# Kernel optimization log

Measured on AMD Instinct MI355X. Metric: run time of the kernel, lower is better.

The kernel has to match this reference:

```python
import jax, jax.numpy as jnp
import numpy as np

DIM = 1024
HEADS = 16
HEAD_DIM = DIM // HEADS


def setup_inputs() -> dict:
    key = jax.random.key(0)
    ks = jax.random.split(key, 7)
    scale = 1.0 / np.sqrt(DIM)
    x = jax.random.normal(ks[0], (2, 2048, DIM), dtype=jnp.float32)
    Wq = jax.random.uniform(ks[1], (DIM, DIM), jnp.float32, -scale, scale)
    bq = jax.random.uniform(ks[2], (DIM,), jnp.float32, -scale, scale)
    Wk = jax.random.uniform(ks[3], (DIM, DIM), jnp.float32, -scale, scale)
    bk = jax.random.uniform(ks[4], (DIM,), jnp.float32, -scale, scale)
    Wv = jax.random.uniform(ks[5], (DIM, DIM), jnp.float32, -scale, scale)
    bv = jax.random.uniform(ks[6], (DIM,), jnp.float32, -scale, scale)
    return {"x": x, "Wq": Wq, "bq": bq, "Wk": Wk, "bk": bk, "Wv": Wv, "bv": bv}


def reference(x, Wq, bq, Wk, bk, Wv, bv):
    b, s, _ = x.shape
    # torch Linear: y = x @ W.T + b
    q = (x @ Wq.T + bq).reshape(b, s, HEADS, HEAD_DIM)
    k = (x @ Wk.T + bk).reshape(b, s, HEADS, HEAD_DIM)
    v = (x @ Wv.T + bv).reshape(b, s, HEADS, HEAD_DIM)
    # scores: (b, s, z, h), softmax over z (key axis = axis 2)
    scores = jnp.einsum('bshd,bzhd->bszh', q, k) / jnp.sqrt(jnp.float32(HEAD_DIM))
    attention = jax.nn.softmax(scores, axis=2)
    output = jnp.einsum('bzhd,bszh->bshd', v, attention)
    return output
```

## Files before the change

kernel.cpp:

```cpp
#include <hip/hip_runtime.h>
#include <hip/hip_bf16.h>

typedef unsigned short u16;
typedef __attribute__((ext_vector_type(8))) __bf16 bf16x8;
typedef __attribute__((ext_vector_type(4))) float f32x4;
typedef __attribute__((ext_vector_type(8))) u16 u16x8;

#define BATCH 2
#define SEQ   2048
#define DIM   1024
#define HEADS 16
#define HDIM  64

#define QSCALE 0.18033688011112042f

__device__ __forceinline__ float bf2f(u16 u) {
  union { unsigned int u; float f; } v; v.u = ((unsigned int)u) << 16; return v.f;
}
__device__ __forceinline__ u16 f2bf(float f) {
  union { float f; unsigned int u; } v; v.f = f;
  unsigned int r = v.u + 0x7fffu + ((v.u >> 16) & 1u);
  return (u16)(r >> 16);
}
__device__ __forceinline__ unsigned int pk2(float a, float b) {
  union { __hip_bfloat162 h2; unsigned int u; } v;
  v.h2 = __float22bfloat162_rn(float2{a, b});
  return v.u;
}

__device__ __forceinline__ void async16(u16* lds, const u16* g) {
  __builtin_amdgcn_global_load_lds(
      (__attribute__((address_space(1))) void*)(void*)(g),
      (__attribute__((address_space(3))) void*)(lds), 16, 0, 0);
}

#define XG  524288
#define WG  131072
extern "C" __global__ __launch_bounds__(256)
void convert_all(const float* __restrict__ x,  const float* __restrict__ wq,
                 const float* __restrict__ wk, const float* __restrict__ wv,
                 u16* __restrict__ xbf, u16* __restrict__ wbf)
{
  const int g = blockIdx.x * 256 + threadIdx.x;
  const float* src; u16* dst; size_t off;
  if (g < XG)               { src = x;  dst = xbf;                 off = (size_t)g; }
  else if (g < XG + WG)     { src = wq; dst = wbf;                 off = (size_t)(g - XG); }
  else if (g < XG + 2 * WG) { src = wk; dst = wbf + DIM * DIM;     off = (size_t)(g - XG - WG); }
  else                      { src = wv; dst = wbf + 2 * DIM * DIM; off = (size_t)(g - XG - 2 * WG); }
  f32x4 a = *(const f32x4*)(src + off * 8);
  f32x4 b = *(const f32x4*)(src + off * 8 + 4);
  u16x8 o;
#pragma unroll
  for (int i = 0; i < 4; ++i) { o[i] = f2bf(a[i]); o[4 + i] = f2bf(b[i]); }
  *(u16x8*)(dst + off * 8) = o;
}

extern "C" __global__ __launch_bounds__(256)
void qkv_gemm(const u16* __restrict__ xbf, const u16* __restrict__ wbf,
              const float* __restrict__ bq, const float* __restrict__ bk,
              const float* __restrict__ bv,
              u16* __restrict__ qo, u16* __restrict__ ko, u16* __restrict__ vto)
{
  __shared__ alignas(16) u16 Albs[128 * 64];
  __shared__ alignas(16) u16 Blbs[128 * 64];

  const int which = blockIdx.z;
  const u16* Wb = wbf + (size_t)which * DIM * DIM;
  const float* bias = (which == 0) ? bq : (which == 1) ? bk : bv;

  const int lane = threadIdx.x & 63;
  const int wave = threadIdx.x >> 6;
  const int l16  = lane & 15;
  const int quad = lane >> 4;
  const int r8   = lane >> 3;
  const int sl   = lane & 7;
  const int jsw  = sl ^ (r8 & 7);
  const int e7   = l16 & 7;

  const int mBase = blockIdx.y * 128;
  const int nBase = blockIdx.x * 128;
  const int mw = (wave >> 1) * 64;
  const int nw = (wave & 1) * 64;

  f32x4 acc[4][4] = {};

  for (int k0 = 0; k0 < DIM; k0 += 64) {
#pragma unroll
    for (int p = 0; p < 4; ++p) {
      const int i = wave * 4 + p;
      async16(&Albs[i * 512], xbf + (size_t)(mBase + i * 8 + r8) * DIM + k0 + jsw * 8);
      async16(&Blbs[i * 512], Wb  + (size_t)(nBase + i * 8 + r8) * DIM + k0 + jsw * 8);
    }
    asm volatile("s_waitcnt vmcnt(0)" ::: "memory");
    __syncthreads();

    bf16x8 af[4][2], bfr[4][2];
#pragma unroll
    for (int i = 0; i < 4; ++i)
#pragma unroll
      for (int ks = 0; ks < 2; ++ks) {
        af[i][ks]  = *(const bf16x8*)&Albs[(mw + i * 16 + l16) * 64 + ((ks * 4 + quad) ^ e7) * 8];
        bfr[i][ks] = *(const bf16x8*)&Blbs[(nw + i * 16 + l16) * 64 + ((ks * 4 + quad) ^ e7) * 8];
      }
#pragma unroll
    for (int ks = 0; ks < 2; ++ks)
#pragma unroll
      for (int mi = 0; mi < 4; ++mi)
#pragma unroll
        for (int ni = 0; ni < 4; ++ni)
          acc[mi][ni] = __builtin_amdgcn_mfma_f32_16x16x32_bf16(af[mi][ks], bfr[ni][ks], acc[mi][ni], 0, 0, 0);
    __syncthreads();
  }

  const float oscale = (which == 0) ? QSCALE : 1.0f;
#pragma unroll
  for (int ni = 0; ni < 4; ++ni) {
    const int n = nBase + nw + ni * 16 + l16;
    const float bval = bias[n];
    const int h = n >> 6, d = n & 63;
#pragma unroll
    for (int mi = 0; mi < 4; ++mi) {
#pragma unroll
      for (int r = 0; r < 4; ++r) {
        const int m = mBase + mw + mi * 16 + quad * 4 + r;
        const int bi = m >> 11, s = m & 2047;
        const u16 val = f2bf((acc[mi][ni][r] + bval) * oscale);
        if (which == 2) {
          vto[((size_t)(bi * HEADS + h) * HDIM + d) * SEQ + s] = val;
        } else {
          u16* dst = (which == 0) ? qo : ko;
          dst[((size_t)(bi * HEADS + h) * SEQ + s) * HDIM + d] = val;
        }
      }
    }
  }
}

extern "C" __global__ __launch_bounds__(256)
void attn(const u16* __restrict__ q, const u16* __restrict__ k,
          const u16* __restrict__ vt, float* __restrict__ out)
{
  __shared__ alignas(16) u16 Klds[3][64 * 64];
  __shared__ alignas(16) u16 Vlds[3][64 * 64];
  __shared__ alignas(16) u16 Plds[4][32 * 64];

  const int lane = threadIdx.x & 63;
  const int wave = threadIdx.x >> 6;
  const int l16  = lane & 15;
  const int quad = lane >> 4;
  const int r8   = lane >> 3;
  const int sl   = lane & 7;
  const int jsw  = sl ^ (r8 & 7);
  const int e7   = l16 & 7;
  const int psw  = e7 * 2;

  const int h     = blockIdx.y;
  const int b     = blockIdx.z;
  const int qbase = blockIdx.x * 128 + wave * 32;

  const u16* qh  = q  + (size_t)(b * HEADS + h) * SEQ * HDIM;
  const u16* kh  = k  + (size_t)(b * HEADS + h) * SEQ * HDIM;
  const u16* vth = vt + (size_t)(b * HEADS + h) * HDIM * SEQ;

  bf16x8 qf[2][2];
#pragma unroll
  for (int qg = 0; qg < 2; ++qg)
#pragma unroll
    for (int ks = 0; ks < 2; ++ks)
      qf[qg][ks] = *(const bf16x8*)(qh + (size_t)(qbase + qg * 16 + l16) * HDIM + ks * 32 + quad * 8);

  float lsum[2] = {};
  f32x4 o[2][4] = {};
  f32x4 sc[2][4] = {};
  u16* pw = &Plds[wave][0];

  auto stage = [&](int bidx, int kb) {
#pragma unroll
    for (int p = 0; p < 2; ++p) {
      const int i = wave * 2 + p;
      async16(&Klds[bidx][i * 512], kh  + (size_t)(kb + i * 8 + r8) * HDIM + jsw * 8);
      async16(&Vlds[bidx][i * 512], vth + (size_t)(i * 8 + r8) * SEQ + kb + jsw * 8);
    }
  };
  auto qkt = [&](int bidx) {
#pragma unroll
    for (int qg = 0; qg < 2; ++qg)
#pragma unroll
      for (int nt = 0; nt < 4; ++nt) sc[qg][nt] = f32x4{0.f, 0.f, 0.f, 0.f};
#pragma unroll
    for (int ks = 0; ks < 2; ++ks)
#pragma unroll
      for (int nt = 0; nt < 4; ++nt) {
        bf16x8 kf = *(const bf16x8*)&Klds[bidx][(nt * 16 + l16) * 64 + ((ks * 4 + quad) ^ e7) * 8];
#pragma unroll
        for (int qg = 0; qg < 2; ++qg)
          sc[qg][nt] = __builtin_amdgcn_mfma_f32_16x16x32_bf16(kf, qf[qg][ks], sc[qg][nt], 0, 0, 0);
      }
  };

  stage(0, 0);
  stage(1, 64);
  asm volatile("s_waitcnt vmcnt(0)" ::: "memory");
  __syncthreads();
  qkt(0);

  int i0 = 0, i1 = 1, i2 = 2;
  for (int t = 0; t < 32; ++t) {
    if (t < 30) stage(i2, (t + 2) * 64);

#pragma unroll
    for (int qg = 0; qg < 2; ++qg) {
      float ls = 0.f;
#pragma unroll
      for (int nt = 0; nt < 4; ++nt) {
        const float p0 = __builtin_exp2f(sc[qg][nt][0]);
        const float p1 = __builtin_exp2f(sc[qg][nt][1]);
        const float p2 = __builtin_exp2f(sc[qg][nt][2]);
        const float p3 = __builtin_exp2f(sc[qg][nt][3]);
        ls += (p0 + p1) + (p2 + p3);
        uint2 pkv; pkv.x = pk2(p0, p1); pkv.y = pk2(p2, p3);
        *(uint2*)(pw + (qg * 16 + l16) * 64 + ((nt * 4 + quad) ^ psw) * 4) = pkv;
      }
      lsum[qg] += ls;
    }

    if (t < 31) qkt(i1);

#pragma unroll
    for (int ks = 0; ks < 2; ++ks) {
      bf16x8 pf0 = *(const bf16x8*)&pw[(0 * 16 + l16) * 64 + ((ks * 8 + quad * 2) ^ psw) * 4];
      bf16x8 pf1 = *(const bf16x8*)&pw[(1 * 16 + l16) * 64 + ((ks * 8 + quad * 2) ^ psw) * 4];
#pragma unroll
      for (int dt = 0; dt < 4; ++dt) {
        bf16x8 vfr = *(const bf16x8*)&Vlds[i0][(dt * 16 + l16) * 64 + ((ks * 4 + quad) ^ e7) * 8];
        o[0][dt] = __builtin_amdgcn_mfma_f32_16x16x32_bf16(pf0, vfr, o[0][dt], 0, 0, 0);
        o[1][dt] = __builtin_amdgcn_mfma_f32_16x16x32_bf16(pf1, vfr, o[1][dt], 0, 0, 0);
      }
    }

    if (t < 31) {
      asm volatile("s_waitcnt vmcnt(0)" ::: "memory");
      __syncthreads();
    }
    const int tmp = i0; i0 = i1; i1 = i2; i2 = tmp;
  }

#pragma unroll
  for (int qg = 0; qg < 2; ++qg) {
    lsum[qg] += __shfl_xor(lsum[qg], 16, 64);
    lsum[qg] += __shfl_xor(lsum[qg], 32, 64);
  }
  asm volatile("s_waitcnt lgkmcnt(0)" ::: "memory");
  float* lw = (float*)pw;
  if (lane < 16) { lw[lane] = lsum[0]; lw[16 + lane] = lsum[1]; }
  asm volatile("s_waitcnt lgkmcnt(0)" ::: "memory");

#pragma unroll
  for (int qg = 0; qg < 2; ++qg) {
#pragma unroll
    for (int r = 0; r < 4; ++r) {
      const float inv = 1.f / fmaxf(lw[qg * 16 + quad * 4 + r], 1e-20f);
      const int s = qbase + qg * 16 + quad * 4 + r;
#pragma unroll
      for (int dt = 0; dt < 4; ++dt) {
        const int d = dt * 16 + l16;
        out[((size_t)(b * SEQ + s) * HEADS + h) * HDIM + d] = o[qg][dt][r] * inv;
      }
    }
  }
}

extern "C" void kernel_launch(void* const* d_in, const int* in_sizes, int n_in,
                              void* d_out, int out_size, void* d_ws, size_t ws_size,
                              hipStream_t stream) {
  (void)in_sizes; (void)n_in; (void)out_size; (void)ws_size;
  const float* x  = (const float*)d_in[0];
  const float* Wq = (const float*)d_in[1];
  const float* bq = (const float*)d_in[2];
  const float* Wk = (const float*)d_in[3];
  const float* bk = (const float*)d_in[4];
  const float* Wv = (const float*)d_in[5];
  const float* bv = (const float*)d_in[6];
  float* out = (float*)d_out;

  u16* ws = (u16*)d_ws;
  const size_t XSZ = (size_t)BATCH * SEQ * DIM;
  const size_t WSZ = (size_t)DIM * DIM;
  const size_t QSZ = (size_t)BATCH * HEADS * SEQ * HDIM;
  u16* xbf   = ws;
  u16* wbf   = ws + XSZ;
  u16* qbuf  = ws + XSZ + 3 * WSZ;
  u16* kbuf  = qbuf + QSZ;
  u16* vtbuf = kbuf + QSZ;

  convert_all<<<3584, 256, 0, stream>>>(x, Wq, Wk, Wv, xbf, wbf);

  dim3 g1(DIM / 128, (BATCH * SEQ) / 128, 3);
  qkv_gemm<<<g1, 256, 0, stream>>>(xbf, wbf, bq, bk, bv, qbuf, kbuf, vtbuf);

  dim3 g2(SEQ / 128, HEADS, BATCH);
  attn<<<g2, 256, 0, stream>>>(qbuf, kbuf, vtbuf, out);
}
```

Measured before the change: 213.3 us.

## Shrink GEMM K-tile, relax attention vmcnt waits, use native exp2, reswizzle P

The QKV GEMM now stages 32-wide K tiles instead of 64-wide, using an unswizzled LDS layout and one MFMA k-step per tile. This halves LDS use but doubles the number of barriers. The attention kernel waits only for the older staged buffer (vmcnt(4)), so the prefetch of the next K/V tile stays in flight across the barrier. It also calls the raw hardware exp2 intrinsic and changes the P-tile LDS swizzle to XOR with l16, reading P as two 8-byte loads to cut bank conflicts. The unswizzled GEMM LDS reads may bring bank conflicts, and the partial vmcnt assumes a fixed count of async loads per stage.

```diff
diff --git a/kernel.cpp b/kernel.cpp
--- a/kernel.cpp
+++ b/kernel.cpp
@@ -61,8 +61,8 @@
               const float* __restrict__ bv,
               u16* __restrict__ qo, u16* __restrict__ ko, u16* __restrict__ vto)
 {
-  __shared__ alignas(16) u16 Albs[128 * 64];
-  __shared__ alignas(16) u16 Blbs[128 * 64];
+  __shared__ alignas(16) u16 Albs[128 * 32];
+  __shared__ alignas(16) u16 Blbs[128 * 32];
 
   const int which = blockIdx.z;
   const u16* Wb = wbf + (size_t)which * DIM * DIM;
@@ -72,10 +72,8 @@
   const int wave = threadIdx.x >> 6;
   const int l16  = lane & 15;
   const int quad = lane >> 4;
-  const int r8   = lane >> 3;
-  const int sl   = lane & 7;
-  const int jsw  = sl ^ (r8 & 7);
-  const int e7   = l16 & 7;
+  const int lrow = lane >> 2;
+  const int lcol = (lane & 3) * 8;
 
   const int mBase = blockIdx.y * 128;
   const int nBase = blockIdx.x * 128;
@@ -84,31 +82,28 @@
 
   f32x4 acc[4][4] = {};
 
-  for (int k0 = 0; k0 < DIM; k0 += 64) {
-#pragma unroll
-    for (int p = 0; p < 4; ++p) {
-      const int i = wave * 4 + p;
-      async16(&Albs[i * 512], xbf + (size_t)(mBase + i * 8 + r8) * DIM + k0 + jsw * 8);
-      async16(&Blbs[i * 512], Wb  + (size_t)(nBase + i * 8 + r8) * DIM + k0 + jsw * 8);
+  for (int k0 = 0; k0 < DIM; k0 += 32) {
+#pragma unroll
+    for (int p = 0; p < 2; ++p) {
+      const int r16 = wave * 2 + p;
+      const int row = r16 * 16 + lrow;
+      async16(&Albs[r16 * 512], xbf + (size_t)(mBase + row) * DIM + k0 + lcol);
+      async16(&Blbs[r16 * 512], Wb  + (size_t)(nBase + row) * DIM + k0 + lcol);
     }
     asm volatile("s_waitcnt vmcnt(0)" ::: "memory");
     __syncthreads();
 
-    bf16x8 af[4][2], bfr[4][2];
-#pragma unroll
-    for (int i = 0; i < 4; ++i)
-#pragma unroll
-      for (int ks = 0; ks < 2; ++ks) {
-        af[i][ks]  = *(const bf16x8*)&Albs[(mw + i * 16 + l16) * 64 + ((ks * 4 + quad) ^ e7) * 8];
-        bfr[i][ks] = *(const bf16x8*)&Blbs[(nw + i * 16 + l16) * 64 + ((ks * 4 + quad) ^ e7) * 8];
-      }
-#pragma unroll
-    for (int ks = 0; ks < 2; ++ks)
-#pragma unroll
-      for (int mi = 0; mi < 4; ++mi)
-#pragma unroll
-        for (int ni = 0; ni < 4; ++ni)
-          acc[mi][ni] = __builtin_amdgcn_mfma_f32_16x16x32_bf16(af[mi][ks], bfr[ni][ks], acc[mi][ni], 0, 0, 0);
+    bf16x8 af[4], bfr[4];
+#pragma unroll
+    for (int i = 0; i < 4; ++i) {
+      af[i]  = *(const bf16x8*)&Albs[(mw + i * 16 + l16) * 32 + quad * 8];
+      bfr[i] = *(const bf16x8*)&Blbs[(nw + i * 16 + l16) * 32 + quad * 8];
+    }
+#pragma unroll
+    for (int mi = 0; mi < 4; ++mi)
+#pragma unroll
+      for (int ni = 0; ni < 4; ++ni)
+        acc[mi][ni] = __builtin_amdgcn_mfma_f32_16x16x32_bf16(af[mi], bfr[ni], acc[mi][ni], 0, 0, 0);
     __syncthreads();
   }
 
@@ -152,7 +147,6 @@
   const int sl   = lane & 7;
   const int jsw  = sl ^ (r8 & 7);
   const int e7   = l16 & 7;
-  const int psw  = e7 * 2;
 
   const int h     = blockIdx.y;
   const int b     = blockIdx.z;
@@ -200,7 +194,7 @@
 
   stage(0, 0);
   stage(1, 64);
-  asm volatile("s_waitcnt vmcnt(0)" ::: "memory");
+  asm volatile("s_waitcnt vmcnt(4)" ::: "memory");
   __syncthreads();
   qkt(0);
 
@@ -213,13 +207,13 @@
       float ls = 0.f;
 #pragma unroll
       for (int nt = 0; nt < 4; ++nt) {
-        const float p0 = __builtin_exp2f(sc[qg][nt][0]);
-        const float p1 = __builtin_exp2f(sc[qg][nt][1]);
-        const float p2 = __builtin_exp2f(sc[qg][nt][2]);
-        const float p3 = __builtin_exp2f(sc[qg][nt][3]);
+        const float p0 = __builtin_amdgcn_exp2f(sc[qg][nt][0]);
+        const float p1 = __builtin_amdgcn_exp2f(sc[qg][nt][1]);
+        const float p2 = __builtin_amdgcn_exp2f(sc[qg][nt][2]);
+        const float p3 = __builtin_amdgcn_exp2f(sc[qg][nt][3]);
         ls += (p0 + p1) + (p2 + p3);
         uint2 pkv; pkv.x = pk2(p0, p1); pkv.y = pk2(p2, p3);
-        *(uint2*)(pw + (qg * 16 + l16) * 64 + ((nt * 4 + quad) ^ psw) * 4) = pkv;
+        *(uint2*)(pw + (qg * 16 + l16) * 64 + (((nt * 4 + quad) ^ l16) * 4)) = pkv;
       }
       lsum[qg] += ls;
     }
@@ -228,20 +222,28 @@
 
 #pragma unroll
     for (int ks = 0; ks < 2; ++ks) {
-      bf16x8 pf0 = *(const bf16x8*)&pw[(0 * 16 + l16) * 64 + ((ks * 8 + quad * 2) ^ psw) * 4];
-      bf16x8 pf1 = *(const bf16x8*)&pw[(1 * 16 + l16) * 64 + ((ks * 8 + quad * 2) ^ psw) * 4];
+      bf16x8 pf[2];
+#pragma unroll
+      for (int qg = 0; qg < 2; ++qg) {
+        const int rowo = (qg * 16 + l16) * 64;
+        const int s0 = ks * 8 + quad * 2;
+        uint2 lo = *(const uint2*)(pw + rowo + ((s0    ) ^ l16) * 4);
+        uint2 hi = *(const uint2*)(pw + rowo + ((s0 + 1) ^ l16) * 4);
+        union { uint4 u; bf16x8 v; } cvt;
+        cvt.u = uint4{lo.x, lo.y, hi.x, hi.y};
+        pf[qg] = cvt.v;
+      }
 #pragma unroll
       for (int dt = 0; dt < 4; ++dt) {
         bf16x8 vfr = *(const bf16x8*)&Vlds[i0][(dt * 16 + l16) * 64 + ((ks * 4 + quad) ^ e7) * 8];
-        o[0][dt] = __builtin_amdgcn_mfma_f32_16x16x32_bf16(pf0, vfr, o[0][dt], 0, 0, 0);
-        o[1][dt] = __builtin_amdgcn_mfma_f32_16x16x32_bf16(pf1, vfr, o[1][dt], 0, 0, 0);
-      }
-    }
-
-    if (t < 31) {
-      asm volatile("s_waitcnt vmcnt(0)" ::: "memory");
-      __syncthreads();
-    }
+        o[0][dt] = __builtin_amdgcn_mfma_f32_16x16x32_bf16(pf[0], vfr, o[0][dt], 0, 0, 0);
+        o[1][dt] = __builtin_amdgcn_mfma_f32_16x16x32_bf16(pf[1], vfr, o[1][dt], 0, 0, 0);
+      }
+    }
+
+    if (t < 30)      asm volatile("s_waitcnt vmcnt(4)" ::: "memory");
+    else if (t < 31) asm volatile("s_waitcnt vmcnt(0)" ::: "memory");
+    if (t < 31) __syncthreads();
     const int tmp = i0; i0 = i1; i1 = i2; i2 = tmp;
   }
 
```

New measurement: 180.3 us. -15.5%, faster.
